# Kernel tuning notes

Hardware: AMD Instinct MI355X
Metric: run time of the kernel (lower is better)

Reference implementation:

```python
import jax, jax.numpy as jnp
import numpy as np

NUM_TAGS = 512
START_TAG = 510
STOP_TAG = 511
NEG_INF = -10000.0
BATCH, SEQ_LEN = 64, 512


def setup_inputs() -> dict:
    key = jax.random.key(0)
    k1, k2, k3 = jax.random.split(key, 3)
    inputs = jax.random.normal(k1, (BATCH, SEQ_LEN, NUM_TAGS), dtype=jnp.float32)
    tags = jax.random.randint(k2, (BATCH, SEQ_LEN), 0, 510)
    transitions = jax.random.normal(k3, (NUM_TAGS, NUM_TAGS), dtype=jnp.float32)
    # faithful to __init__: start row and stop column clamped to -10000
    transitions = transitions.at[START_TAG, :].set(NEG_INF).at[:, STOP_TAG].set(NEG_INF)
    return {"inputs": inputs, "tags": tags, "transitions": transitions}


def _lse_source(x):
    # Faithful to the source's log_sum_exp: it subtracts the max but never
    # adds it back, i.e. returns logsumexp(x) - max(x) over the last dim.
    return jax.nn.logsumexp(x, axis=-1) - jnp.max(x, axis=-1)


def _log_denominator(inputs, transitions):
    B, L, T = inputs.shape
    fv0 = jnp.full((B, T), NEG_INF, dtype=inputs.dtype).at[:, START_TAG].set(0.0)

    def step(fv, emit_t):  # fv [B, T_prev], emit_t [B, T_next]
        # scores[b, next, prev] = fv[b, prev] + trans[next, prev] + emit[b, next]
        scores = fv[:, None, :] + transitions[None, :, :] + emit_t[:, :, None]
        return _lse_source(scores), None

    fv, _ = jax.lax.scan(step, fv0, jnp.transpose(inputs, (1, 0, 2)))
    terminal = fv + transitions[STOP_TAG][None, :]
    return _lse_source(terminal)  # [B]


def _log_numerator(inputs, tags, transitions):
    B, L, T = inputs.shape
    score = transitions[tags[:, 0], START_TAG]  # start -> first tag
    # transitions between consecutive tags: trans[tags[:, i+1], tags[:, i]]
    trans_scores = transitions[tags[:, 1:], tags[:, :-1]]  # [B, L-1]
    # emission: faithful to source, uses inputs at position i with tag at i+1
    emit_scores = jnp.take_along_axis(
        inputs[:, :-1, :], tags[:, 1:, None], axis=2
    )[..., 0]  # [B, L-1]
    score = score + jnp.sum(trans_scores + emit_scores, axis=1)
    score = score + transitions[STOP_TAG, tags[:, -1]]
    return score  # [B]


def reference(inputs, tags, transitions):
    log_den = _log_denominator(inputs, transitions)
    log_num = _log_numerator(inputs, tags, transitions)
    return jnp.sum(log_num - log_den)
```

## Files before the change

kernel.cpp:

```cpp
#include <hip/hip_runtime.h>
#include <math.h>
#include <stdint.h>

#define NTAGS 512
#define SEQL  512
#define BATCH 64
#define START_TAG 510
#define STOP_TAG  511
#define NEG_INF  -10000.0f

#define NB   64
#define BT   512
#define ROWS (NTAGS / NB)

#define WS_NUM_OFF  0
#define WS_SLOT_OFF 256
#define WS_BYTES    (WS_SLOT_OFF + 2 * NTAGS * 8)

#define AGLD(p) __hip_atomic_load((p), __ATOMIC_RELAXED, __HIP_MEMORY_SCOPE_AGENT)

__global__ __launch_bounds__(BT) void crf_fused(
    const float* __restrict__ inputs, const int* __restrict__ tags,
    const float* __restrict__ trans, void* __restrict__ ws,
    float* __restrict__ out)
{
    __shared__ float t_lds[ROWS * NTAGS];
    __shared__ float fv_lds[2][NTAGS];

    const int tid   = threadIdx.x;
    const int bid   = blockIdx.x;
    const int lane  = tid & 63;
    const int wave  = tid >> 6;
    const int myrow = bid * ROWS + wave;

    float*    numacc = (float*)((char*)ws + WS_NUM_OFF);
    uint64_t* slots  = (uint64_t*)((char*)ws + WS_SLOT_OFF);

    {
        const float4* src = (const float4*)(trans + (size_t)bid * ROWS * NTAGS);
        float4*       dst = (float4*)t_lds;
        dst[tid]      = src[tid];
        dst[tid + BT] = src[tid + BT];
    }

    float ns;
    {
        const int*   tg  = tags + bid * SEQL;
        const float* inb = inputs + (size_t)bid * SEQL * NTAGS;
        if (tid > 0) {
            const int cur = tg[tid], prev = tg[tid - 1];
            ns = trans[cur * NTAGS + prev] + inb[(size_t)(tid - 1) * NTAGS + cur];
        } else {
            ns = trans[tg[0] * NTAGS + START_TAG] + trans[STOP_TAG * NTAGS + tg[SEQL - 1]];
        }
    }
    #pragma unroll
    for (int off = 32; off; off >>= 1) ns += __shfl_xor(ns, off);
    if (lane == 0) atomicAdd(numacc, ns);
    __builtin_amdgcn_s_waitcnt(0);

    fv_lds[0][tid] = (tid == START_TAG) ? 0.0f : NEG_INF;
    __syncthreads();

    const float* tr = t_lds + wave * NTAGS;

    float mprev = (myrow == START_TAG) ? NEG_INF : 0.0f;

    for (int s = 0; s < SEQL; ++s) {
        const int pp = (s + 1) & 1;
        uint64_t* buf = slots + (unsigned)pp * NTAGS;
        uint64_t* myslot = &buf[tid];
        const unsigned want = (unsigned)(s + 1);
        const float* fvc = fv_lds[s & 1];

        uint64_t p = AGLD(myslot);

        float v[8];
        #pragma unroll
        for (int q = 0; q < 8; ++q)
            v[q] = fvc[lane + 64 * q] + tr[lane + 64 * q];

        float m = fmaxf(fmaxf(fmaxf(v[0], v[1]), fmaxf(v[2], v[3])),
                        fmaxf(fmaxf(v[4], v[5]), fmaxf(v[6], v[7])));
        float ss = ((__expf(v[0] - mprev) + __expf(v[1] - mprev))
                  + (__expf(v[2] - mprev) + __expf(v[3] - mprev)))
                 + ((__expf(v[4] - mprev) + __expf(v[5] - mprev))
                  + (__expf(v[6] - mprev) + __expf(v[7] - mprev)));

        #pragma unroll
        for (int off = 32; off; off >>= 1) {
            const float ms  = __shfl_xor(m, off);
            const float sss = __shfl_xor(ss, off);
            m  = fmaxf(m, ms);
            ss += sss;
        }

        if (lane == 0) {
            const float nv = __logf(ss) + mprev - m;
            const uint64_t pk = ((uint64_t)want << 32) | (uint64_t)__float_as_uint(nv);
            __hip_atomic_store(&buf[myrow], pk, __ATOMIC_RELAXED, __HIP_MEMORY_SCOPE_AGENT);
        }
        mprev = m;

        if ((unsigned)(p >> 32) != want) {
            uint64_t q0 = AGLD(myslot), q1 = AGLD(myslot),
                     q2 = AGLD(myslot), q3 = AGLD(myslot);
            for (;;) {
                if ((unsigned)(q0 >> 32) == want) { p = q0; break; }
                q0 = AGLD(myslot);
                if ((unsigned)(q1 >> 32) == want) { p = q1; break; }
                q1 = AGLD(myslot);
                if ((unsigned)(q2 >> 32) == want) { p = q2; break; }
                q2 = AGLD(myslot);
                if ((unsigned)(q3 >> 32) == want) { p = q3; break; }
                q3 = AGLD(myslot);
            }
        }
        fv_lds[pp][tid] = __uint_as_float((unsigned)(p & 0xFFFFFFFFu));
        __syncthreads();
    }

    if (myrow == STOP_TAG) {
        const float* fvf = fv_lds[0];
        float v[8];
        #pragma unroll
        for (int q = 0; q < 8; ++q)
            v[q] = fvf[lane + 64 * q] + tr[lane + 64 * q];
        float m = fmaxf(fmaxf(fmaxf(v[0], v[1]), fmaxf(v[2], v[3])),
                        fmaxf(fmaxf(v[4], v[5]), fmaxf(v[6], v[7])));
        float ss = ((__expf(v[0]) + __expf(v[1])) + (__expf(v[2]) + __expf(v[3])))
                 + ((__expf(v[4]) + __expf(v[5])) + (__expf(v[6]) + __expf(v[7])));
        #pragma unroll
        for (int off = 32; off; off >>= 1) {
            const float ms  = __shfl_xor(m, off);
            const float sss = __shfl_xor(ss, off);
            m  = fmaxf(m, ms);
            ss += sss;
        }
        if (lane == 0) {
            const float ld  = __logf(ss) - m;
            const float num = AGLD(numacc);
            out[0] = num - (float)BATCH * ld;
        }
    }
}

extern "C" void kernel_launch(void* const* d_in, const int* in_sizes, int n_in,
                              void* d_out, int out_size, void* d_ws, size_t ws_size,
                              hipStream_t stream)
{
    const float* inputs = (const float*)d_in[0];
    const int*   tags   = (const int*)  d_in[1];
    const float* trans  = (const float*)d_in[2];
    float* out = (float*)d_out;

    hipMemsetAsync(d_ws, 0, WS_BYTES, stream);

    crf_fused<<<NB, BT, 0, stream>>>(inputs, tags, trans, d_ws, out);
}
```

Baseline: 889.8 us.

## Use 16 blocks of 1024 threads with two transition rows per wave

Reduces the persistent grid from 64 to 16 blocks. Each block holds 32 transition rows in LDS and each wave computes two rows per step, sharing the forward-vector loads between them. This cuts the number of blocks that must exchange slots through global memory each timestep and reduces cross-block polling traffic. In exchange each wave does twice the exp work per step, and only half the threads poll slots. The numerator partial sums are first reduced per block in LDS, so each block issues a single atomic.

```diff
diff --git a/kernel.cpp b/kernel.cpp
--- a/kernel.cpp
+++ b/kernel.cpp
@@ -9,9 +9,11 @@
 #define STOP_TAG  511
 #define NEG_INF  -10000.0f
 
-#define NB   64
-#define BT   512
-#define ROWS (NTAGS / NB)
+#define NB    16
+#define BT    1024
+#define WAVES 16
+#define ROWS  32
+#define BPB   4
 
 #define WS_NUM_OFF  0
 #define WS_SLOT_OFF 256
@@ -26,12 +28,13 @@
 {
     __shared__ float t_lds[ROWS * NTAGS];
     __shared__ float fv_lds[2][NTAGS];
+    __shared__ float nred[WAVES];
 
-    const int tid   = threadIdx.x;
-    const int bid   = blockIdx.x;
-    const int lane  = tid & 63;
-    const int wave  = tid >> 6;
-    const int myrow = bid * ROWS + wave;
+    const int tid  = threadIdx.x;
+    const int bid  = blockIdx.x;
+    const int lane = tid & 63;
+    const int wave = tid >> 6;
+    const int r0   = bid * ROWS + wave * 2;
 
     float*    numacc = (float*)((char*)ws + WS_NUM_OFF);
     uint64_t* slots  = (uint64_t*)((char*)ws + WS_SLOT_OFF);
@@ -39,93 +42,124 @@
     {
         const float4* src = (const float4*)(trans + (size_t)bid * ROWS * NTAGS);
         float4*       dst = (float4*)t_lds;
-        dst[tid]      = src[tid];
-        dst[tid + BT] = src[tid + BT];
+        #pragma unroll
+        for (int k = 0; k < ROWS * NTAGS / 4 / BT; ++k)
+            dst[tid + k * BT] = src[tid + k * BT];
     }
 
-    float ns;
+    float ns = 0.0f;
     {
-        const int*   tg  = tags + bid * SEQL;
-        const float* inb = inputs + (size_t)bid * SEQL * NTAGS;
-        if (tid > 0) {
-            const int cur = tg[tid], prev = tg[tid - 1];
-            ns = trans[cur * NTAGS + prev] + inb[(size_t)(tid - 1) * NTAGS + cur];
-        } else {
-            ns = trans[tg[0] * NTAGS + START_TAG] + trans[STOP_TAG * NTAGS + tg[SEQL - 1]];
+        const int sub = tid >> 9;
+        const int pos = tid & 511;
+        #pragma unroll
+        for (int bb = 0; bb < 2; ++bb) {
+            const int b = bid * BPB + bb * 2 + sub;
+            const int*   tg  = tags + b * SEQL;
+            const float* inb = inputs + (size_t)b * SEQL * NTAGS;
+            if (pos > 0) {
+                const int cur = tg[pos], prev = tg[pos - 1];
+                ns += trans[cur * NTAGS + prev] + inb[(size_t)(pos - 1) * NTAGS + cur];
+            } else {
+                ns += trans[tg[0] * NTAGS + START_TAG] + trans[STOP_TAG * NTAGS + tg[SEQL - 1]];
+            }
         }
     }
     #pragma unroll
     for (int off = 32; off; off >>= 1) ns += __shfl_xor(ns, off);
-    if (lane == 0) atomicAdd(numacc, ns);
-    __builtin_amdgcn_s_waitcnt(0);
+    if (lane == 0) nred[wave] = ns;
 
-    fv_lds[0][tid] = (tid == START_TAG) ? 0.0f : NEG_INF;
+    if (tid < NTAGS) fv_lds[0][tid] = (tid == START_TAG) ? 0.0f : NEG_INF;
     __syncthreads();
+    if (tid == 0) {
+        float t = 0.0f;
+        #pragma unroll
+        for (int i = 0; i < WAVES; ++i) t += nred[i];
+        atomicAdd(numacc, t);
+    }
 
-    const float* tr = t_lds + wave * NTAGS;
+    const float* trA = t_lds + (size_t)(wave * 2 + 0) * NTAGS;
+    const float* trB = trA + NTAGS;
 
-    float mprev = (myrow == START_TAG) ? NEG_INF : 0.0f;
+    float mprevA = (r0     == START_TAG) ? NEG_INF : 0.0f;
+    float mprevB = (r0 + 1 == START_TAG) ? NEG_INF : 0.0f;
 
     for (int s = 0; s < SEQL; ++s) {
         const int pp = (s + 1) & 1;
         uint64_t* buf = slots + (unsigned)pp * NTAGS;
-        uint64_t* myslot = &buf[tid];
         const unsigned want = (unsigned)(s + 1);
         const float* fvc = fv_lds[s & 1];
 
-        uint64_t p = AGLD(myslot);
+        uint64_t p = 0;
+        if (tid < NTAGS) p = AGLD(&buf[tid]);
 
-        float v[8];
+        float f[8], vA[8], vB[8];
         #pragma unroll
-        for (int q = 0; q < 8; ++q)
-            v[q] = fvc[lane + 64 * q] + tr[lane + 64 * q];
-
-        float m = fmaxf(fmaxf(fmaxf(v[0], v[1]), fmaxf(v[2], v[3])),
-                        fmaxf(fmaxf(v[4], v[5]), fmaxf(v[6], v[7])));
-        float ss = ((__expf(v[0] - mprev) + __expf(v[1] - mprev))
-                  + (__expf(v[2] - mprev) + __expf(v[3] - mprev)))
-                 + ((__expf(v[4] - mprev) + __expf(v[5] - mprev))
-                  + (__expf(v[6] - mprev) + __expf(v[7] - mprev)));
+        for (int q = 0; q < 8; ++q) {
+            f[q]  = fvc[lane + 64 * q];
+            vA[q] = f[q] + trA[lane + 64 * q];
+            vB[q] = f[q] + trB[lane + 64 * q];
+        }
+        float mA = fmaxf(fmaxf(fmaxf(vA[0], vA[1]), fmaxf(vA[2], vA[3])),
+                         fmaxf(fmaxf(vA[4], vA[5]), fmaxf(vA[6], vA[7])));
+        float mB = fmaxf(fmaxf(fmaxf(vB[0], vB[1]), fmaxf(vB[2], vB[3])),
+                         fmaxf(fmaxf(vB[4], vB[5]), fmaxf(vB[6], vB[7])));
+        float ssA = ((__expf(vA[0] - mprevA) + __expf(vA[1] - mprevA))
+                   + (__expf(vA[2] - mprevA) + __expf(vA[3] - mprevA)))
+                  + ((__expf(vA[4] - mprevA) + __expf(vA[5] - mprevA))
+                   + (__expf(vA[6] - mprevA) + __expf(vA[7] - mprevA)));
+        float ssB = ((__expf(vB[0] - mprevB) + __expf(vB[1] - mprevB))
+                   + (__expf(vB[2] - mprevB) + __expf(vB[3] - mprevB)))
+                  + ((__expf(vB[4] - mprevB) + __expf(vB[5] - mprevB))
+                   + (__expf(vB[6] - mprevB) + __expf(vB[7] - mprevB)));
 
         #pragma unroll
         for (int off = 32; off; off >>= 1) {
-            const float ms  = __shfl_xor(m, off);
-            const float sss = __shfl_xor(ss, off);
-            m  = fmaxf(m, ms);
-            ss += sss;
+            const float a1 = __shfl_xor(mA, off);
+            const float a2 = __shfl_xor(ssA, off);
+            const float b1 = __shfl_xor(mB, off);
+            const float b2 = __shfl_xor(ssB, off);
+            mA = fmaxf(mA, a1); ssA += a2;
+            mB = fmaxf(mB, b1); ssB += b2;
         }
 
-        if (lane == 0) {
-            const float nv = __logf(ss) + mprev - m;
-            const uint64_t pk = ((uint64_t)want << 32) | (uint64_t)__float_as_uint(nv);
-            __hip_atomic_store(&buf[myrow], pk, __ATOMIC_RELAXED, __HIP_MEMORY_SCOPE_AGENT);
-        }
-        mprev = m;
-
-        if ((unsigned)(p >> 32) != want) {
-            uint64_t q0 = AGLD(myslot), q1 = AGLD(myslot),
-                     q2 = AGLD(myslot), q3 = AGLD(myslot);
-            for (;;) {
-                if ((unsigned)(q0 >> 32) == want) { p = q0; break; }
-                q0 = AGLD(myslot);
-                if ((unsigned)(q1 >> 32) == want) { p = q1; break; }
-                q1 = AGLD(myslot);
-                if ((unsigned)(q2 >> 32) == want) { p = q2; break; }
-                q2 = AGLD(myslot);
-                if ((unsigned)(q3 >> 32) == want) { p = q3; break; }
-                q3 = AGLD(myslot);
+        {
+            const float nvA = __logf(ssA) + mprevA - mA;
+            const float nvB = __logf(ssB) + mprevB - mB;
+            if (lane < 2) {
+                const float nv = lane ? nvB : nvA;
+                const uint64_t pk = ((uint64_t)want << 32) | (uint64_t)__float_as_uint(nv);
+                __hip_atomic_store(&buf[r0 + lane], pk, __ATOMIC_RELAXED, __HIP_MEMORY_SCOPE_AGENT);
             }
         }
-        fv_lds[pp][tid] = __uint_as_float((unsigned)(p & 0xFFFFFFFFu));
+        mprevA = mA; mprevB = mB;
+
+        if (tid < NTAGS) {
+            uint64_t* myslot = &buf[tid];
+            if ((unsigned)(p >> 32) != want) {
+                uint64_t q0 = AGLD(myslot), q1 = AGLD(myslot),
+                         q2 = AGLD(myslot), q3 = AGLD(myslot);
+                for (;;) {
+                    if ((unsigned)(q0 >> 32) == want) { p = q0; break; }
+                    q0 = AGLD(myslot);
+                    if ((unsigned)(q1 >> 32) == want) { p = q1; break; }
+                    q1 = AGLD(myslot);
+                    if ((unsigned)(q2 >> 32) == want) { p = q2; break; }
+                    q2 = AGLD(myslot);
+                    if ((unsigned)(q3 >> 32) == want) { p = q3; break; }
+                    q3 = AGLD(myslot);
+                }
+            }
+            fv_lds[pp][tid] = __uint_as_float((unsigned)(p & 0xFFFFFFFFu));
+        }
         __syncthreads();
     }
 
-    if (myrow == STOP_TAG) {
+    if (bid == NB - 1 && wave == WAVES - 1) {
         const float* fvf = fv_lds[0];
         float v[8];
         #pragma unroll
         for (int q = 0; q < 8; ++q)
-            v[q] = fvf[lane + 64 * q] + tr[lane + 64 * q];
+            v[q] = fvf[lane + 64 * q] + trB[lane + 64 * q];
         float m = fmaxf(fmaxf(fmaxf(v[0], v[1]), fmaxf(v[2], v[3])),
                         fmaxf(fmaxf(v[4], v[5]), fmaxf(v[6], v[7])));
         float ss = ((__expf(v[0]) + __expf(v[1])) + (__expf(v[2]) + __expf(v[3])))
```

New measurement: 2.030 ms. +128.1%, slower.

## Replicate published forward-vector slots and keep transition rows in registers

Applied to the files above, without the earlier changes.

Each wave now writes its new forward-variable value into eight replicated slot arrays, one store per lane, and each block polls the replica chosen by its block index. This spreads the cross-block polling traffic of 64 blocks over eight copies instead of all of them hitting one array. The transition row is also held in registers instead of shared memory, which removes an LDS read per step. The cost is eight times more global stores per step and a larger workspace.

```diff
diff --git a/kernel.cpp b/kernel.cpp
--- a/kernel.cpp
+++ b/kernel.cpp
@@ -11,11 +11,12 @@
 
 #define NB   64
 #define BT   512
-#define ROWS (NTAGS / NB)
+#define ROWS 8
+#define REPS 8
 
 #define WS_NUM_OFF  0
 #define WS_SLOT_OFF 256
-#define WS_BYTES    (WS_SLOT_OFF + 2 * NTAGS * 8)
+#define WS_BYTES    (WS_SLOT_OFF + 2 * REPS * NTAGS * 8)
 
 #define AGLD(p) __hip_atomic_load((p), __ATOMIC_RELAXED, __HIP_MEMORY_SCOPE_AGENT)
 
@@ -24,7 +25,6 @@
     const float* __restrict__ trans, void* __restrict__ ws,
     float* __restrict__ out)
 {
-    __shared__ float t_lds[ROWS * NTAGS];
     __shared__ float fv_lds[2][NTAGS];
 
     const int tid   = threadIdx.x;
@@ -32,15 +32,16 @@
     const int lane  = tid & 63;
     const int wave  = tid >> 6;
     const int myrow = bid * ROWS + wave;
+    const int rep   = bid & (REPS - 1);
 
     float*    numacc = (float*)((char*)ws + WS_NUM_OFF);
     uint64_t* slots  = (uint64_t*)((char*)ws + WS_SLOT_OFF);
 
+    float treg[8];
     {
-        const float4* src = (const float4*)(trans + (size_t)bid * ROWS * NTAGS);
-        float4*       dst = (float4*)t_lds;
-        dst[tid]      = src[tid];
-        dst[tid + BT] = src[tid + BT];
+        const float* trow = trans + (size_t)myrow * NTAGS;
+        #pragma unroll
+        for (int q = 0; q < 8; ++q) treg[q] = trow[lane + 64 * q];
     }
 
     float ns;
@@ -62,14 +63,12 @@
     fv_lds[0][tid] = (tid == START_TAG) ? 0.0f : NEG_INF;
     __syncthreads();
 
-    const float* tr = t_lds + wave * NTAGS;
-
     float mprev = (myrow == START_TAG) ? NEG_INF : 0.0f;
 
     for (int s = 0; s < SEQL; ++s) {
         const int pp = (s + 1) & 1;
-        uint64_t* buf = slots + (unsigned)pp * NTAGS;
-        uint64_t* myslot = &buf[tid];
+        uint64_t* pubbase = slots + (size_t)pp * REPS * NTAGS;
+        uint64_t* myslot  = slots + ((size_t)pp * REPS + rep) * NTAGS + tid;
         const unsigned want = (unsigned)(s + 1);
         const float* fvc = fv_lds[s & 1];
 
@@ -78,7 +77,7 @@
         float v[8];
         #pragma unroll
         for (int q = 0; q < 8; ++q)
-            v[q] = fvc[lane + 64 * q] + tr[lane + 64 * q];
+            v[q] = fvc[lane + 64 * q] + treg[q];
 
         float m = fmaxf(fmaxf(fmaxf(v[0], v[1]), fmaxf(v[2], v[3])),
                         fmaxf(fmaxf(v[4], v[5]), fmaxf(v[6], v[7])));
@@ -95,10 +94,12 @@
             ss += sss;
         }
 
-        if (lane == 0) {
+        {
             const float nv = __logf(ss) + mprev - m;
             const uint64_t pk = ((uint64_t)want << 32) | (uint64_t)__float_as_uint(nv);
-            __hip_atomic_store(&buf[myrow], pk, __ATOMIC_RELAXED, __HIP_MEMORY_SCOPE_AGENT);
+            if (lane < REPS)
+                __hip_atomic_store(pubbase + (size_t)lane * NTAGS + myrow, pk,
+                                   __ATOMIC_RELAXED, __HIP_MEMORY_SCOPE_AGENT);
         }
         mprev = m;
 
@@ -125,7 +126,7 @@
         float v[8];
         #pragma unroll
         for (int q = 0; q < 8; ++q)
-            v[q] = fvf[lane + 64 * q] + tr[lane + 64 * q];
+            v[q] = fvf[lane + 64 * q] + treg[q];
         float m = fmaxf(fmaxf(fmaxf(v[0], v[1]), fmaxf(v[2], v[3])),
                         fmaxf(fmaxf(v[4], v[5]), fmaxf(v[6], v[7])));
         float ss = ((__expf(v[0]) + __expf(v[1])) + (__expf(v[2]) + __expf(v[3])))
```

After: 833.4 us. 1.07x faster.
